# Kernel tuning notes

Measured on AMD Instinct MI355X. Metric: run time of the kernel, lower is better.

Reference implementation:

```python
import jax, jax.numpy as jnp
import numpy as np

# module config (matches init_kwargs)
EMBED = 128; HEADS = 8; HEAD_DIM = EMBED // HEADS  # 16, power of 2
MODES = 16            # hardcoded in FuncSelfAttention
WS = 4                # window_size
SHIFT = 2             # shift_size
NSUB = 8              # n_sub (subdomain grid of the full image)
NW = (NSUB // WS) ** 2   # 4 windows per image
S = WS * WS              # 16 tokens (subdomains) per window
BATCH0 = 4; B = BATCH0 * NW  # 16
P = 32                # per-subdomain spatial resolution (needs P//2+1 >= MODES)
HID = 512             # LogCPB MLP hidden width (Swin-v2 style)


def win_decompose2d(x, nsx, nsy, ws):
    # x: [b, c, H, W] -> [(b*wx*wy), ws*ws, c, sh, sw]
    b, c, H, W = x.shape
    sh = H // nsx; sw = W // nsy
    wx = nsx // ws; wy = nsy // ws
    x = x.reshape(b, c, wx, ws, sh, wy, ws, sw)
    x = x.transpose(0, 2, 5, 3, 6, 1, 4, 7)  # b, wx, wy, qx, qy, c, sh, sw
    return x.reshape(b * wx * wy, ws * ws, c, sh, sw)


def win_recompose2d(x, nsx, nsy, ws):
    # inverse of win_decompose2d: [(b*wx*wy), ws*ws, c, sh, sw] -> [b, c, H, W]
    wx = nsx // ws; wy = nsy // ws
    Bn, s, c, sh, sw = x.shape
    b = Bn // (wx * wy)
    x = x.reshape(b, wx, wy, ws, ws, c, sh, sw)
    x = x.transpose(0, 5, 1, 3, 6, 2, 4, 7)
    return x.reshape(b, c, wx * ws * sh, wy * ws * sw)


def spectral_conv(x, wr, wi):
    # SimpleSpectralConv2d: rfft2 -> low-mode complex channel mixing -> irfft2
    # x: [b, s, cin, h, w]; wr/wi: [cin, cout, m, m]
    m = wr.shape[-1]
    h, w = x.shape[-2:]
    xf = jnp.fft.rfft2(x, axes=(-2, -1))                       # [b,s,cin,h,w//2+1]
    ym = jnp.einsum('bsixy,ioxy->bsoxy', xf[..., :m, :m], wr + 1j * wi)
    out_ft = jnp.zeros(x.shape[:2] + (wr.shape[1], h, w // 2 + 1), dtype=ym.dtype)
    out_ft = out_ft.at[..., :m, :m].set(ym)
    return jnp.fft.irfft2(out_ft, s=(h, w), axes=(-2, -1))


def log_cpb(ws, w1, b1, w2):
    # Swin-v2 style log-spaced continuous position bias MLP -> [heads, S, S]
    g = jnp.arange(ws)
    coords = jnp.stack(jnp.meshgrid(g, g, indexing='ij'), -1).reshape(-1, 2)  # [S,2]
    rel = (coords[:, None, :] - coords[None, :, :]).astype(jnp.float32)       # [S,S,2]
    rel = jnp.sign(rel) * jnp.log2(1.0 + jnp.abs(rel)) / jnp.log2(8.0) * 8.0
    hdn = jax.nn.relu(rel @ w1 + b1)
    return (hdn @ w2).transpose(2, 0, 1)


def _build_attn_mask():
    # Faithful port of the Swin shifted-window mask construction in __init__
    img = np.zeros((NSUB, NSUB), np.float32)
    sl = [slice(0, -WS), slice(-WS, -SHIFT), slice(-SHIFT, None)]
    cnt = 0
    for hs in sl:
        for ws_ in sl:
            img[hs, ws_] = cnt
            cnt += 1
    mw = img.reshape(NSUB // WS, WS, NSUB // WS, WS).transpose(0, 2, 1, 3).reshape(NW, S)
    diff = mw[:, None, :] - mw[:, :, None]
    m = np.where(diff != 0, -1e9, 0.0).astype(np.float32)      # -inf in torch; -1e9 for safe grads
    return np.broadcast_to(m[:, None, :, :], (NW, HEADS, S, S)).copy()


def setup_inputs():
    key = jax.random.key(0)
    ks = jax.random.split(key, 8)
    sc = 1.0 / EMBED
    return {
        'seq': jax.random.normal(ks[0], (B, S, EMBED, P, P), jnp.float32),
        'qkv_wr': jax.random.normal(ks[1], (EMBED, 3 * EMBED, MODES, MODES), jnp.float32) * sc,
        'qkv_wi': jax.random.normal(ks[2], (EMBED, 3 * EMBED, MODES, MODES), jnp.float32) * sc,
        'out_wr': jax.random.normal(ks[3], (EMBED, EMBED, MODES, MODES), jnp.float32) * sc,
        'out_wi': jax.random.normal(ks[4], (EMBED, EMBED, MODES, MODES), jnp.float32) * sc,
        'cpb_w1': jax.random.normal(ks[5], (2, HID), jnp.float32) * 0.1,
        'cpb_b1': jnp.zeros((HID,), jnp.float32),
        'cpb_w2': jax.random.normal(ks[6], (HID, HEADS), jnp.float32) * 0.05,
        'attn_mask': jnp.asarray(_build_attn_mask()),
    }


def reference(seq, qkv_wr, qkv_wi, out_wr, out_wi, cpb_w1, cpb_b1, cpb_w2, attn_mask):
    Bn, s, C, h, w = seq.shape
    ssx = w // WS; ssy = h // WS  # subdomain_size per code: seq.size(-1)//n_sub_x with n_sub_x=window_size
    # shift: recompose windows to images, roll, decompose back
    x = win_recompose2d(seq, WS, WS, WS)
    x = jnp.roll(x, (-SHIFT * ssx, -SHIFT * ssy), axis=(-2, -1))
    x = win_decompose2d(x, WS, WS, WS)
    # qkv = spectral conv + residual tiling (v.repeat with dims[2]=3)
    qkv = spectral_conv(x, qkv_wr, qkv_wi) + jnp.concatenate([x, x, x], axis=2)
    qkv = qkv.reshape(Bn, s, 3, HEADS, HEAD_DIM, h, w)
    q = qkv[:, :, 0].transpose(0, 2, 1, 3, 4, 5)  # [B, H, s, d, h, w]
    k = qkv[:, :, 1].transpose(0, 2, 1, 3, 4, 5)
    v = qkv[:, :, 2].transpose(0, 2, 1, 3, 4, 5)
    bias = attn_mask + log_cpb(WS, cpb_w1, cpb_b1, cpb_w2)[None]  # [nW, H, S, S]
    # 'reimann' scores: Riemann-sum (mean over grid) inner product of q_i, k_j functions
    scale = 1.0 / ((h * w) * jnp.sqrt(jnp.float32(HEAD_DIM)))
    scores = jnp.einsum('bnidxy,bnjdxy->bnij', q, k) * scale      # [B, H, S, S]
    scores = scores.reshape(Bn // NW, NW, HEADS, s, s) + bias[None]
    attn = jax.nn.softmax(scores, axis=-1).reshape(Bn, HEADS, s, s)
    sa = jnp.einsum('bnij,bnjdxy->bnidxy', attn, v)               # [B, H, S, d, h, w]
    sa = sa.transpose(0, 2, 1, 3, 4, 5).reshape(Bn, s, C, h, w)   # _flatten
    sa = spectral_conv(sa, out_wr, out_wi)
    # un-shift
    sa = win_recompose2d(sa, WS, WS, WS)
    sa = jnp.roll(sa, (SHIFT * ssx, SHIFT * ssy), axis=(-2, -1))
    return win_decompose2d(sa, WS, WS, WS)
```

## Files before the change

kernel.cpp:

```cpp
#include <hip/hip_runtime.h>
#include <hip/hip_bf16.h>
#include <math.h>


#define DEVI __device__ __forceinline__
typedef unsigned short u16;
typedef unsigned int u32;
typedef __attribute__((ext_vector_type(8))) short short8;
typedef __attribute__((ext_vector_type(4))) float f32x4;

DEVI u16 f2b(float f) {
  union { __hip_bfloat16 h; u16 u; } cv;
  cv.h = __float2bfloat16(f);
  return cv.u;
}
DEVI float b2f(u16 u) { return __uint_as_float(((u32)u) << 16); }

__global__ __launch_bounds__(256) void k_bias(
    const float* __restrict__ w1, const float* __restrict__ b1,
    const float* __restrict__ w2, const float* __restrict__ amask,
    float* __restrict__ biasb) {
  __shared__ float w1s[1024];
  __shared__ float b1s[512];
  __shared__ float w2s[4096];
  int t = threadIdx.x;
  for (int k = t; k < 1024; k += 256) w1s[k] = w1[k];
  for (int k = t; k < 512; k += 256) b1s[k] = b1[k];
  for (int k = t; k < 4096; k += 256) w2s[k] = w2[k];
  __syncthreads();
  int i = t >> 4, j = t & 15;
  float r0 = (float)((i >> 2) - (j >> 2));
  float r1 = (float)((i & 3) - (j & 3));
  const float sc = 8.0f / 3.0f;
  float f0 = (r0 == 0.f) ? 0.f : copysignf(log2f(1.f + fabsf(r0)) * sc, r0);
  float f1 = (r1 == 0.f) ? 0.f : copysignf(log2f(1.f + fabsf(r1)) * sc, r1);
  float o[8];
#pragma unroll
  for (int h = 0; h < 8; h++) o[h] = 0.f;
  for (int k = 0; k < 512; k++) {
    float hd = f0 * w1s[k] + f1 * w1s[512 + k] + b1s[k];
    hd = fmaxf(hd, 0.f);
#pragma unroll
    for (int h = 0; h < 8; h++) o[h] += hd * w2s[k * 8 + h];
  }
  for (int w = 0; w < 4; w++)
#pragma unroll
    for (int h = 0; h < 8; h++) {
      int idx = ((w * 8 + h) * 16 + i) * 16 + j;
      biasb[idx] = amask[idx] + o[h];
    }
}

__global__ __launch_bounds__(256) void k_transpose_wb(
    const float* __restrict__ wr, const float* __restrict__ wi,
    ushort2* __restrict__ dst, int N) {
  __shared__ ushort2 ld[256][17];
  int t = threadIdx.x;
  int ob = blockIdx.x * 16;
  int cb = blockIdx.y * 8;
  for (int cc = 0; cc < 8; cc++) {
    int c = cb + cc;
    for (int oo = 0; oo < 16; oo++) {
      size_t si = ((size_t)c * N + ob + oo) * 256 + t;
      ushort2 u;
      u.x = f2b(wr[si]);
      u.y = f2b(wi[si]);
      ld[t][oo] = u;
    }
    __syncthreads();
    {
      int oo = t & 15, tq = t >> 4;
#pragma unroll
      for (int mr = 0; mr < 16; mr++) {
        int m = mr * 16 + tq;
        dst[((size_t)m * 128 + c) * N + ob + oo] = ld[m][oo];
      }
    }
    __syncthreads();
  }
}

template <int N>
__global__ __launch_bounds__(256) void k_build_b(
    const ushort2* __restrict__ Ws1, u16* __restrict__ Bt) {
  __shared__ ushort2 tile[128][65];
  int t = threadIdx.x;
  int ob = blockIdx.x;
  int m = blockIdx.y;
  {
    int c4 = t >> 6, o = t & 63;
    for (int cc = 0; cc < 32; cc++) {
      int c = cc * 4 + c4;
      tile[c][o] = Ws1[((size_t)m * 128 + c) * N + ob * 64 + o];
    }
  }
  __syncthreads();
  int l = t & 63, w2 = t >> 6;
  for (int rr = 0; rr < 32; rr++) {
    int r = w2 * 32 + rr;
    int ol = r >> 1, p = r & 1;
    size_t rowoff = ((size_t)m * (2 * N) + (size_t)ob * 128 + r) * 256;
#pragma unroll
    for (int ch = 0; ch < 2; ch++) {
      int c = ch * 64 + l;
      ushort2 wv = tile[c][ol];
      ushort2 u;
      u.x = p ? wv.y : wv.x;
      u.y = p ? wv.x : (u16)(wv.y ^ 0x8000);
      *(ushort2*)(Bt + rowoff + 2 * c) = u;
    }
  }
}

__global__ __launch_bounds__(256) void k_build_wdft(u16* __restrict__ Wdft) {
  int n = blockIdx.x;
  int m = n >> 1, q = n & 1;
  int kx = m >> 4, ky = m & 15;
  int t = threadIdx.x;
#pragma unroll
  for (int i = 0; i < 4; i++) {
    int p = i * 256 + t;
    int u = p >> 5, v = p & 31;
    int ph = (kx * u + ky * v) & 31;
    float th = 6.283185307179586f * (float)ph / 32.f;
    float sv, cv;
    sincosf(th, &sv, &cv);
    Wdft[(size_t)n * 1024 + p] = f2b(q ? -sv : cv);
  }
}

__global__ __launch_bounds__(256) void k_build_widft(u16* __restrict__ Widf) {
  int p = blockIdx.x;
  int x = p >> 5, y = p & 31;
  for (int n = threadIdx.x; n < 512; n += 256) {
    int m = n >> 1, q = n & 1;
    int kx = m >> 4, ky = m & 15;
    int ph = (kx * x + ky * y) & 31;
    float th = 6.283185307179586f * (float)ph / 32.f;
    float sv, cv;
    sincosf(th, &sv, &cv);
    float cky = (ky == 0) ? (1.f / 1024.f) : (2.f / 1024.f);
    Widf[(size_t)p * 512 + n] = f2b(q ? -sv * cky : cv * cky);
  }
}

__global__ __launch_bounds__(256) void k_gather(
    const float* __restrict__ seq, u16* __restrict__ Tbf) {
  int t = threadIdx.x;
  int cq = blockIdx.x;
  int bs = blockIdx.y;
  int b = bs >> 4, s = bs & 15;
  int qx = s >> 2, qy = s & 3;
  int u = t >> 3, vb = (t & 7) * 4;
  int uu = u + 16;
  int u2 = uu & 31;
  int qx2 = (qx + (uu >> 5)) & 3;
  int vv = vb + 16;
  int v2 = vv & 31;
  int qy2 = (qy + (vv >> 5)) & 3;
  int s2 = qx2 * 4 + qy2;
  size_t srcbase = (((size_t)(b * 16 + s2) * 128) << 10) + u2 * 32 + v2;
  size_t dstbase = (((size_t)bs * 128) << 10) + u * 32 + vb;
  for (int cc = 0; cc < 32; cc++) {
    size_t coff = (size_t)(cq * 32 + cc) << 10;
    float4 v = *(const float4*)(seq + srcbase + coff);
    ushort4 o;
    o.x = f2b(v.x);
    o.y = f2b(v.y);
    o.z = f2b(v.z);
    o.w = f2b(v.w);
    *(ushort4*)(Tbf + dstbase + coff) = o;
  }
}

__global__ __launch_bounds__(512) void k_dftm(
    const u16* __restrict__ Wdft, const u16* __restrict__ Tbf,
    float2* __restrict__ Xlow, u16* __restrict__ Xbf) {
  __shared__ char As[32768];
  __shared__ char Bs[16384];
  int t = threadIdx.x;
  int mt = blockIdx.x, bs = blockIdx.y;
  int l = t & 63, w = t >> 6;
  int wm = w >> 1, wn = w & 1;
  f32x4 acc[4][4];
#pragma unroll
  for (int a_ = 0; a_ < 4; a_++)
#pragma unroll
    for (int b_ = 0; b_ < 4; b_++) acc[a_][b_] = (f32x4){0.f, 0.f, 0.f, 0.f};
  const u16* Ab = Wdft + (size_t)mt * 256 * 1024;
  const u16* Bb = Tbf + (size_t)bs * 128 * 1024;
  int srow = t >> 3, ss = t & 7;
  uint4 ra[4], rb[2];
#pragma unroll
  for (int i = 0; i < 4; i++)
    ra[i] = *(const uint4*)(Ab + (size_t)(i * 64 + srow) * 1024 + ss * 8);
#pragma unroll
  for (int i = 0; i < 2; i++)
    rb[i] = *(const uint4*)(Bb + (size_t)(i * 64 + srow) * 1024 + ss * 8);
  for (int kt = 0; kt < 16; kt++) {
    if (kt) __syncthreads();
#pragma unroll
    for (int i = 0; i < 4; i++) {
      int row = i * 64 + srow;
      *(uint4*)(As + row * 128 + ((ss ^ (row & 7)) << 4)) = ra[i];
    }
#pragma unroll
    for (int i = 0; i < 2; i++) {
      int row = i * 64 + srow;
      *(uint4*)(Bs + row * 128 + ((ss ^ (row & 7)) << 4)) = rb[i];
    }
    if (kt < 15) {
#pragma unroll
      for (int i = 0; i < 4; i++)
        ra[i] = *(const uint4*)(Ab + (size_t)(i * 64 + srow) * 1024 +
                                (kt + 1) * 64 + ss * 8);
#pragma unroll
      for (int i = 0; i < 2; i++)
        rb[i] = *(const uint4*)(Bb + (size_t)(i * 64 + srow) * 1024 +
                                (kt + 1) * 64 + ss * 8);
    }
    __syncthreads();
#pragma unroll
    for (int kk = 0; kk < 2; kk++) {
      short8 af[4], bg[4];
#pragma unroll
      for (int fm = 0; fm < 4; fm++) {
        int row = wm * 64 + fm * 16 + (l & 15);
        int chunk = kk * 4 + (l >> 4);
        af[fm] = *(const short8*)(As + row * 128 + ((chunk ^ (row & 7)) << 4));
      }
#pragma unroll
      for (int fn = 0; fn < 4; fn++) {
        int row = wn * 64 + fn * 16 + (l & 15);
        int chunk = kk * 4 + (l >> 4);
        bg[fn] = *(const short8*)(Bs + row * 128 + ((chunk ^ (row & 7)) << 4));
      }
#pragma unroll
      for (int fm = 0; fm < 4; fm++)
#pragma unroll
        for (int fn = 0; fn < 4; fn++)
          acc[fm][fn] = __builtin_amdgcn_mfma_f32_16x16x32_bf16(
              af[fm], bg[fn], acc[fm][fn], 0, 0, 0);
    }
  }
  int cr = (l >> 4) * 4, ccol = l & 15;
#pragma unroll
  for (int fm = 0; fm < 4; fm++) {
    int nbase = mt * 256 + wm * 64 + fm * 16 + cr;
#pragma unroll
    for (int fn = 0; fn < 4; fn++) {
      int c = wn * 64 + fn * 16 + ccol;
#pragma unroll
      for (int rp = 0; rp < 4; rp += 2) {
        int n0 = nbase + rp;
        size_t row = (size_t)(n0 >> 1) * 256 + bs;
        float v0 = acc[fm][fn][rp], v1 = acc[fm][fn][rp + 1];
        Xlow[row * 128 + c] = make_float2(v0, v1);
        ushort2 ub;
        ub.x = f2b(v0);
        ub.y = f2b(v1);
        *(ushort2*)(Xbf + row * 256 + 2 * c) = ub;
      }
    }
  }
}

__global__ __launch_bounds__(64) void k_gram_mfma(
    const u16* __restrict__ Tbf, float* __restrict__ Gpart) {
  int dc = blockIdx.x;
  int bh = blockIdx.y;
  int b = bh >> 3, h = bh & 7;
  int l = threadIdx.x;
  f32x4 a0 = (f32x4){0.f, 0.f, 0.f, 0.f};
  f32x4 a1 = (f32x4){0.f, 0.f, 0.f, 0.f};
  const u16* base =
      Tbf + ((size_t)(b * 16 + (l & 15)) * 128 + h * 16 + dc * 4) * 1024;
  int ko = (l >> 4) * 8;
  for (int kk = 0; kk < 128; kk += 2) {
    short8 f0 = *(const short8*)(base + kk * 32 + ko);
    short8 f1 = *(const short8*)(base + kk * 32 + 32 + ko);
    a0 = __builtin_amdgcn_mfma_f32_16x16x32_bf16(f0, f0, a0, 0, 0, 0);
    a1 = __builtin_amdgcn_mfma_f32_16x16x32_bf16(f1, f1, a1, 0, 0, 0);
  }
  float* dst = Gpart + ((size_t)(dc * 16 + b) * 8 + h) * 256;
#pragma unroll
  for (int r = 0; r < 4; r++)
    dst[((l >> 4) * 4 + r) * 16 + (l & 15)] = a0[r] + a1[r];
}

template <int NP>
__global__ __launch_bounds__(512) void k_mixm(
    const u16* __restrict__ A, const u16* __restrict__ Bm,
    u16* __restrict__ Cb) {
  __shared__ char lds[65536];
  char* As = lds;
  char* Bs = lds + 32768;
  u16* st = (u16*)lds;
  int t = threadIdx.x;
  const int gx = NP / 256;
  int orig = blockIdx.y * gx + blockIdx.x;
  const int tot = gx * 256;
  int lid = (orig & 7) * (tot >> 3) + (orig >> 3);
  int nt = lid % gx;
  int m = lid / gx;
  int l = t & 63, w = t >> 6;
  int wm = w >> 1, wn = w & 1;
  f32x4 acc[4][8];
#pragma unroll
  for (int a_ = 0; a_ < 4; a_++)
#pragma unroll
    for (int b_ = 0; b_ < 8; b_++) acc[a_][b_] = (f32x4){0.f, 0.f, 0.f, 0.f};
  const u16* Ab = A + (size_t)m * 256 * 256;
  const u16* Bb = Bm + ((size_t)m * NP + nt * 256) * 256;
  int srow = t >> 3, ss = t & 7;
  uint4 ra[4], rb[4];
#pragma unroll
  for (int i = 0; i < 4; i++) {
    int row = i * 64 + srow;
    ra[i] = *(const uint4*)(Ab + (size_t)row * 256 + ss * 8);
    rb[i] = *(const uint4*)(Bb + (size_t)row * 256 + ss * 8);
  }
  for (int kt = 0; kt < 4; kt++) {
    if (kt) __syncthreads();
#pragma unroll
    for (int i = 0; i < 4; i++) {
      int row = i * 64 + srow;
      int sw = ((ss ^ (row & 7)) << 4);
      *(uint4*)(As + row * 128 + sw) = ra[i];
      *(uint4*)(Bs + row * 128 + sw) = rb[i];
    }
    if (kt < 3) {
#pragma unroll
      for (int i = 0; i < 4; i++) {
        int row = i * 64 + srow;
        ra[i] =
            *(const uint4*)(Ab + (size_t)row * 256 + (kt + 1) * 64 + ss * 8);
        rb[i] =
            *(const uint4*)(Bb + (size_t)row * 256 + (kt + 1) * 64 + ss * 8);
      }
    }
    __syncthreads();
#pragma unroll
    for (int kk = 0; kk < 2; kk++) {
      short8 af[4], bg[8];
#pragma unroll
      for (int fm = 0; fm < 4; fm++) {
        int row = wm * 64 + fm * 16 + (l & 15);
        int chunk = kk * 4 + (l >> 4);
        af[fm] = *(const short8*)(As + row * 128 + ((chunk ^ (row & 7)) << 4));
      }
#pragma unroll
      for (int fn = 0; fn < 8; fn++) {
        int row = wn * 128 + fn * 16 + (l & 15);
        int chunk = kk * 4 + (l >> 4);
        bg[fn] = *(const short8*)(Bs + row * 128 + ((chunk ^ (row & 7)) << 4));
      }
#pragma unroll
      for (int fm = 0; fm < 4; fm++)
#pragma unroll
        for (int fn = 0; fn < 8; fn++)
          acc[fm][fn] = __builtin_amdgcn_mfma_f32_16x16x32_bf16(
              bg[fn], af[fm], acc[fm][fn], 0, 0, 0);
    }
  }
#pragma unroll
  for (int fm = 0; fm < 4; fm++) {
    __syncthreads();
    int rloc = wm * 16 + (l & 15);
#pragma unroll
    for (int fn = 0; fn < 8; fn++) {
      int col = wn * 128 + fn * 16 + (l >> 4) * 4;
      ushort4 u;
      u.x = f2b(acc[fm][fn][0]);
      u.y = f2b(acc[fm][fn][1]);
      u.z = f2b(acc[fm][fn][2]);
      u.w = f2b(acc[fm][fn][3]);
      *(ushort4*)(st + rloc * 264 + col) = u;
    }
    __syncthreads();
#pragma unroll
    for (int it = 0; it < 4; it++) {
      int idx = it * 512 + t;
      int row = idx >> 5;
      int ch = idx & 31;
      uint4 v = *(const uint4*)(st + row * 264 + ch * 8);
      int bs = (row >> 4) * 64 + fm * 16 + (row & 15);
      *(uint4*)(Cb + ((size_t)m * 256 + bs) * NP + nt * 256 + ch * 8) = v;
    }
  }
}

__global__ __launch_bounds__(256) void k_transp_out(
    const ushort2* __restrict__ OUTb2, ushort2* __restrict__ OUTt2) {
  __shared__ ushort2 ld[128][129];
  int t = threadIdx.x;
  int bs = blockIdx.x;
  for (int mh = 0; mh < 2; mh++) {
    if (mh) __syncthreads();
    {
      int cidx = t & 127;
      int rb = t >> 7;
      for (int pass = 0; pass < 64; pass++) {
        int r = pass * 2 + rb;
        ld[r][cidx] = OUTb2[((size_t)(mh * 128 + r) * 256 + bs) * 128 + cidx];
      }
    }
    __syncthreads();
    {
      int ml = t & 127;
      int cb = t >> 7;
      for (int pass = 0; pass < 64; pass++) {
        int c = pass * 2 + cb;
        OUTt2[((size_t)bs * 128 + c) * 256 + mh * 128 + ml] = ld[ml][c];
      }
    }
  }
}

__global__ __launch_bounds__(512) void k_irfftm(
    const u16* __restrict__ Widf, const u16* __restrict__ OUTt,
    float* __restrict__ tmp) {
  __shared__ char lds[65536];
  char* As = lds;
  char* Bs = lds + 32768;
  float* stg = (float*)lds;
  int t = threadIdx.x;
  int ph = blockIdx.x, bs = blockIdx.y;
  int l = t & 63, w = t >> 6;
  int wm = w >> 1, wn = w & 1;
  f32x4 acc[4][4];
#pragma unroll
  for (int a_ = 0; a_ < 4; a_++)
#pragma unroll
    for (int b_ = 0; b_ < 4; b_++) acc[a_][b_] = (f32x4){0.f, 0.f, 0.f, 0.f};
  const u16* Ab = Widf + (size_t)ph * 256 * 512;
  const u16* Bb = OUTt + (size_t)bs * 128 * 512;
  int srow = t >> 3, ss = t & 7;
  uint4 ra[4], rb[2];
#pragma unroll
  for (int i = 0; i < 4; i++)
    ra[i] = *(const uint4*)(Ab + (size_t)(i * 64 + srow) * 512 + ss * 8);
#pragma unroll
  for (int i = 0; i < 2; i++)
    rb[i] = *(const uint4*)(Bb + (size_t)(i * 64 + srow) * 512 + ss * 8);
  for (int kt = 0; kt < 8; kt++) {
    if (kt) __syncthreads();
#pragma unroll
    for (int i = 0; i < 4; i++) {
      int row = i * 64 + srow;
      *(uint4*)(As + row * 128 + ((ss ^ (row & 7)) << 4)) = ra[i];
    }
#pragma unroll
    for (int i = 0; i < 2; i++) {
      int row = i * 64 + srow;
      *(uint4*)(Bs + row * 128 + ((ss ^ (row & 7)) << 4)) = rb[i];
    }
    if (kt < 7) {
#pragma unroll
      for (int i = 0; i < 4; i++)
        ra[i] = *(const uint4*)(Ab + (size_t)(i * 64 + srow) * 512 +
                                (kt + 1) * 64 + ss * 8);
#pragma unroll
      for (int i = 0; i < 2; i++)
        rb[i] = *(const uint4*)(Bb + (size_t)(i * 64 + srow) * 512 +
                                (kt + 1) * 64 + ss * 8);
    }
    __syncthreads();
#pragma unroll
    for (int kk = 0; kk < 2; kk++) {
      short8 wf[4], bg[4];
#pragma unroll
      for (int fm = 0; fm < 4; fm++) {
        int row = wm * 64 + fm * 16 + (l & 15);
        int chunk = kk * 4 + (l >> 4);
        wf[fm] = *(const short8*)(As + row * 128 + ((chunk ^ (row & 7)) << 4));
      }
#pragma unroll
      for (int fn = 0; fn < 4; fn++) {
        int row = wn * 64 + fn * 16 + (l & 15);
        int chunk = kk * 4 + (l >> 4);
        bg[fn] = *(const short8*)(Bs + row * 128 + ((chunk ^ (row & 7)) << 4));
      }
#pragma unroll
      for (int fm = 0; fm < 4; fm++)
#pragma unroll
        for (int fn = 0; fn < 4; fn++)
          acc[fm][fn] = __builtin_amdgcn_mfma_f32_16x16x32_bf16(
              wf[fm], bg[fn], acc[fm][fn], 0, 0, 0);
    }
  }
  for (int fmp = 0; fmp < 2; fmp++) {
    __syncthreads();
#pragma unroll
    for (int s = 0; s < 2; s++) {
      int fm = fmp * 2 + s;
#pragma unroll
      for (int fn = 0; fn < 4; fn++) {
        int c = wn * 64 + fn * 16 + (l & 15);
        int row = c * 4 + wm;
        int chunk = (s * 4 + (l >> 4)) ^ (c & 7);
        *(float4*)(stg + (row * 8 + chunk) * 4) =
            make_float4(acc[fm][fn][0], acc[fm][fn][1], acc[fm][fn][2],
                        acc[fm][fn][3]);
      }
    }
    __syncthreads();
#pragma unroll
    for (int it = 0; it < 8; it++) {
      int ci = it * 512 + t;
      int row = ci >> 3, k = ci & 7;
      int c = row >> 2, wm2 = row & 3;
      float4 v = *(const float4*)(stg + (row * 8 + (k ^ (c & 7))) * 4);
      int p0 = ph * 256 + wm2 * 64 + fmp * 32 + k * 4;
      *(float4*)(tmp + (((size_t)(bs * 128 + c)) << 10) + p0) = v;
    }
  }
}

__global__ __launch_bounds__(256) void k_unshift(
    const float* __restrict__ tmp, float* __restrict__ out) {
  int t = threadIdx.x;
  int cq = blockIdx.x;
  int bs2 = blockIdx.y;
  int b = bs2 >> 4, s2 = bs2 & 15;
  int qx2 = s2 >> 2, qy2 = s2 & 3;
  int v2 = (t & 7) * 4;
  int y, qy;
  if (v2 < 16) {
    y = v2 + 16;
    qy = (qy2 + 3) & 3;
  } else {
    y = v2 - 16;
    qy = qy2;
  }
  for (int it = 0; it < 32; it++) {
    int row = it * 32 + (t >> 3);
    int c = cq * 32 + (row >> 5);
    int u2 = row & 31;
    int x, qx;
    if (u2 < 16) {
      x = u2 + 16;
      qx = (qx2 + 3) & 3;
    } else {
      x = u2 - 16;
      qx = qx2;
    }
    int bs_src = b * 16 + qx * 4 + qy;
    float4 v = *(const float4*)(tmp + (((size_t)(bs_src * 128 + c)) << 10) +
                                x * 32 + y);
    *(float4*)(out + (((size_t)(bs2 * 128 + c)) << 10) + u2 * 32 + v2) = v;
  }
}

__global__ __launch_bounds__(256) void k_scores(
    const float2* __restrict__ Xlow, const ushort2* __restrict__ QKVmb,
    float* __restrict__ Spart) {
  __shared__ float2 Xs[16][17], Qs[16][17], Ks[16][17];
  int t = threadIdx.x;
  int mc = blockIdx.x;
  int bh = blockIdx.y;
  int b = bh >> 3, h = bh & 7;
  int i = t >> 4, j = t & 15;
  int bs = b * 16 + i;
  int d = j;
  int m0 = mc * 32;
  size_t xoff = ((size_t)m0 * 256 + bs) * 128 + h * 16 + d;
  size_t qoff = ((size_t)m0 * 256 + bs) * 384 + h * 16 + d;
  float2 px = Xlow[xoff];
  ushort2 uq = QKVmb[qoff];
  ushort2 uk = QKVmb[qoff + 128];
  float acc = 0.f;
  for (int mm = 0; mm < 32; mm++) {
    int m = m0 + mm;
    Xs[i][d] = px;
    Qs[i][d] = make_float2(b2f(uq.x), b2f(uq.y));
    Ks[i][d] = make_float2(b2f(uk.x), b2f(uk.y));
    __syncthreads();
    if (mm < 31) {
      px = Xlow[xoff + (size_t)(mm + 1) * 32768];
      uq = QKVmb[qoff + (size_t)(mm + 1) * 98304];
      uk = QKVmb[qoff + (size_t)(mm + 1) * 98304 + 128];
    }
    int ky = m & 15, kx = m >> 4;
    if (ky > 0) {
#pragma unroll
      for (int dd = 0; dd < 16; dd++) {
        float2 Xi = Xs[i][dd], Qi = Qs[i][dd], Xj = Xs[j][dd], Kj = Ks[j][dd];
        float qr = Xi.x + Qi.x, qi = Xi.y + Qi.y;
        float kr = Xj.x + Kj.x, ki = Xj.y + Kj.y;
        acc += 2.f * (qr * kr + qi * ki - (Xi.x * Xj.x + Xi.y * Xj.y));
      }
    } else {
#pragma unroll
      for (int dd = 0; dd < 16; dd++) {
        float2 Xi = Xs[i][dd], Qi = Qs[i][dd], Xj = Xs[j][dd], Kj = Ks[j][dd];
        float cr = Xi.x * Kj.x + Xi.y * Kj.y + Qi.x * Xj.x + Qi.y * Xj.y;
        float qk =
            (kx == 0) ? (Qi.x * Kj.x) : 0.5f * (Qi.x * Kj.x + Qi.y * Kj.y);
        acc += cr + qk;
      }
    }
    __syncthreads();
  }
  Spart[((size_t)mc * 128 + bh) * 256 + t] = acc;
}

__global__ __launch_bounds__(256) void k_softmax(
    const float* __restrict__ Spart, const float* __restrict__ Gpart,
    const float* __restrict__ biasb, float* __restrict__ attn) {
  int t = threadIdx.x;
  int bh = blockIdx.x;
  int b = bh >> 3, h = bh & 7;
  int i = t >> 4, j = t & 15;
  float acc = 0.f;
#pragma unroll
  for (int mc = 0; mc < 8; mc++)
    acc += Spart[((size_t)mc * 128 + bh) * 256 + t];
  float G = 0.f;
#pragma unroll
  for (int dc = 0; dc < 4; dc++)
    G += Gpart[((size_t)(dc * 16 + b) * 8 + h) * 256 + t];
  float score = G * (1.f / 4096.f) + acc * (1.f / 4194304.f) +
                biasb[(((b & 3) * 8 + h) * 16 + i) * 16 + j];
  float mx = score;
#pragma unroll
  for (int o = 8; o >= 1; o >>= 1) mx = fmaxf(mx, __shfl_xor(mx, o, 16));
  float e = expf(score - mx);
  float sm = e;
#pragma unroll
  for (int o = 8; o >= 1; o >>= 1) sm += __shfl_xor(sm, o, 16);
  attn[(size_t)bh * 256 + t] = e / sm;
}

__global__ __launch_bounds__(256) void k_sav(
    const float2* __restrict__ Xlow, const ushort2* __restrict__ QKVmb,
    const float* __restrict__ attn, ushort2* __restrict__ SAfb) {
  __shared__ float at[8][16][17];
  __shared__ float2 vt[16][130];
  int t = threadIdx.x;
  int mc = blockIdx.x;
  int b = blockIdx.y;
  {
    int h = t >> 5, ii = (t >> 1) & 15, jb = (t & 1) * 8;
#pragma unroll
    for (int k = 0; k < 8; k++)
      at[h][ii][jb + k] = attn[((size_t)(b * 8 + h) * 16 + ii) * 16 + jb + k];
  }
  __syncthreads();
  int i = t >> 4, cg = t & 15;
  for (int mm = 0; mm < 16; mm++) {
    int m = mc * 16 + mm;
    int ky = m & 15, kx = m >> 4;
    {
      int jj = t >> 4;
      size_t row = (size_t)m * 256 + b * 16 + jj;
#pragma unroll
      for (int u = 0; u < 8; u++) {
        int c = cg + u * 16;
        ushort2 uv = QKVmb[row * 384 + 256 + c];
        float2 vm = make_float2(b2f(uv.x), b2f(uv.y));
        float2 xv = Xlow[row * 128 + c];
        float2 vh;
        if (ky == 0) {
          if (kx == 0)
            vh = make_float2(xv.x + vm.x, xv.y);
          else
            vh = make_float2(xv.x + 0.5f * vm.x, xv.y + 0.5f * vm.y);
        } else
          vh = make_float2(xv.x + vm.x, xv.y + vm.y);
        vt[jj][c] = vh;
      }
    }
    __syncthreads();
    float2 o8[8];
#pragma unroll
    for (int u = 0; u < 8; u++) o8[u] = make_float2(0.f, 0.f);
#pragma unroll
    for (int jj = 0; jj < 16; jj++) {
#pragma unroll
      for (int u = 0; u < 8; u++) {
        float av = at[u][i][jj];
        float2 v = vt[jj][cg + u * 16];
        o8[u].x += av * v.x;
        o8[u].y += av * v.y;
      }
    }
    size_t orow = (size_t)m * 256 + b * 16 + i;
#pragma unroll
    for (int u = 0; u < 8; u++) {
      ushort2 ub;
      ub.x = f2b(o8[u].x);
      ub.y = f2b(o8[u].y);
      SAfb[orow * 128 + cg + u * 16] = ub;
    }
    __syncthreads();
  }
}

extern "C" void kernel_launch(void* const* d_in, const int* in_sizes, int n_in,
                              void* d_out, int out_size, void* d_ws,
                              size_t ws_size, hipStream_t stream) {
  (void)in_sizes;
  (void)n_in;
  const float* seq = (const float*)d_in[0];
  const float* qwr = (const float*)d_in[1];
  const float* qwi = (const float*)d_in[2];
  const float* owr = (const float*)d_in[3];
  const float* owi = (const float*)d_in[4];
  const float* cw1 = (const float*)d_in[5];
  const float* cb1 = (const float*)d_in[6];
  const float* cw2 = (const float*)d_in[7];
  const float* amask = (const float*)d_in[8];
  float* out = (float*)d_out;
  char* ws = (char*)d_ws;

  const size_t R = 100663296;
  ushort2* Wq_s1b = (ushort2*)ws;
  u16* Tbf = (u16*)ws;
  u16* Xbf = (u16*)(ws + 67108864);
  u16* Wob = (u16*)ws;
  ushort2* QKVmb = (ushort2*)(ws + R);
  u16* OUTb = (u16*)(ws + R);
  u16* OUTt = (u16*)(ws + R + 33554432);
  float* tmpb = (float*)(ws + R + 2 * 33554432);
  u16* Wqb = (u16*)(ws + 2 * R);
  ushort2* SAfb = (ushort2*)(ws + 2 * R);
  ushort2* Wo_s1b = (ushort2*)(ws + 3 * R);
  float2* Xlow = (float2*)(ws + 3 * R + 16777216);
  char* sm = ws + 3 * R + 16777216 + 67108864;
  u16* Wdft = (u16*)sm;
  float* Gpart = (float*)(sm + 1048576);
  float* biasb = (float*)(sm + 1572864);
  float* attn = (float*)(sm + 1605632);
  float* Spart = (float*)(sm + 1736704);
  u16* Widf = (u16*)(sm + 2785280);
  size_t need = 3 * R + 16777216 + 67108864 + 2785280 + 1048576;

  if (ws_size < need) {
    hipMemsetAsync(d_out, 0, (size_t)out_size * 4, stream);
    return;
  }

  dim3 blk(256);
  k_transpose_wb<<<dim3(24, 16), blk, 0, stream>>>(qwr, qwi, Wq_s1b, 384);
  k_build_b<384><<<dim3(6, 256), blk, 0, stream>>>(Wq_s1b, Wqb);
  k_transpose_wb<<<dim3(8, 16), blk, 0, stream>>>(owr, owi, Wo_s1b, 128);
  k_bias<<<dim3(1), blk, 0, stream>>>(cw1, cb1, cw2, amask, biasb);
  k_build_wdft<<<dim3(512), blk, 0, stream>>>(Wdft);
  k_build_widft<<<dim3(1024), blk, 0, stream>>>(Widf);
  k_gather<<<dim3(4, 256), blk, 0, stream>>>(seq, Tbf);
  k_dftm<<<dim3(2, 256), dim3(512), 0, stream>>>(Wdft, Tbf, Xlow, Xbf);
  k_gram_mfma<<<dim3(4, 128), dim3(64), 0, stream>>>(Tbf, Gpart);
  k_mixm<768><<<dim3(3, 256), dim3(512), 0, stream>>>(Xbf, Wqb, (u16*)QKVmb);
  k_scores<<<dim3(8, 128), blk, 0, stream>>>(Xlow, QKVmb, Spart);
  k_softmax<<<dim3(128), blk, 0, stream>>>(Spart, Gpart, biasb, attn);
  k_build_b<128><<<dim3(2, 256), blk, 0, stream>>>(Wo_s1b, Wob);
  k_sav<<<dim3(16, 16), blk, 0, stream>>>(Xlow, QKVmb, attn, SAfb);
  k_mixm<256><<<dim3(1, 256), dim3(512), 0, stream>>>((const u16*)SAfb, Wob,
                                                      OUTb);
  k_transp_out<<<dim3(256), blk, 0, stream>>>((const ushort2*)OUTb,
                                              (ushort2*)OUTt);
  k_irfftm<<<dim3(4, 256), dim3(512), 0, stream>>>(Widf, OUTt, tmpb);
  k_unshift<<<dim3(4, 256), blk, 0, stream>>>(tmpb, out);
}
```

Before: 844.0 us.

## Drop fp32 Xlow buffer and stage DFT output through LDS for coalesced stores

The DFT kernel no longer writes a separate fp32 complex Xlow array. It writes only the bf16 Xbf, staged through shared memory in two passes so global stores become 16-byte coalesced rows. The scores and S·V kernels now read the bf16 copy and convert it on the fly, which cuts write and read traffic for that intermediate. The cost is lower precision for the residual X term in the scores and values, plus extra barriers in the DFT epilogue.

```diff
diff --git a/kernel.cpp b/kernel.cpp
--- a/kernel.cpp
+++ b/kernel.cpp
@@ -175,9 +175,11 @@
 
 __global__ __launch_bounds__(512) void k_dftm(
     const u16* __restrict__ Wdft, const u16* __restrict__ Tbf,
-    float2* __restrict__ Xlow, u16* __restrict__ Xbf) {
-  __shared__ char As[32768];
-  __shared__ char Bs[16384];
+    u16* __restrict__ Xbf) {
+  __shared__ char lds[49152];
+  char* As = lds;
+  char* Bs = lds + 32768;
+  u16* st = (u16*)lds;
   int t = threadIdx.x;
   int mt = blockIdx.x, bs = blockIdx.y;
   int l = t & 63, w = t >> 6;
@@ -244,23 +246,34 @@
     }
   }
   int cr = (l >> 4) * 4, ccol = l & 15;
-#pragma unroll
-  for (int fm = 0; fm < 4; fm++) {
-    int nbase = mt * 256 + wm * 64 + fm * 16 + cr;
-#pragma unroll
-    for (int fn = 0; fn < 4; fn++) {
-      int c = wn * 64 + fn * 16 + ccol;
-#pragma unroll
-      for (int rp = 0; rp < 4; rp += 2) {
-        int n0 = nbase + rp;
-        size_t row = (size_t)(n0 >> 1) * 256 + bs;
-        float v0 = acc[fm][fn][rp], v1 = acc[fm][fn][rp + 1];
-        Xlow[row * 128 + c] = make_float2(v0, v1);
-        ushort2 ub;
-        ub.x = f2b(v0);
-        ub.y = f2b(v1);
-        *(ushort2*)(Xbf + row * 256 + 2 * c) = ub;
-      }
+  for (int pass = 0; pass < 2; pass++) {
+    __syncthreads();
+    if ((wm >> 1) == pass) {
+#pragma unroll
+      for (int fm = 0; fm < 4; fm++) {
+#pragma unroll
+        for (int fn = 0; fn < 4; fn++) {
+          int c = wn * 64 + fn * 16 + ccol;
+#pragma unroll
+          for (int rp = 0; rp < 4; rp += 2) {
+            int rloc = (wm & 1) * 32 + fm * 8 + ((cr + rp) >> 1);
+            ushort2 ub;
+            ub.x = f2b(acc[fm][fn][rp]);
+            ub.y = f2b(acc[fm][fn][rp + 1]);
+            *(ushort2*)(st + rloc * 264 + 2 * c) = ub;
+          }
+        }
+      }
+    }
+    __syncthreads();
+#pragma unroll
+    for (int it = 0; it < 4; it++) {
+      int idx = it * 512 + t;
+      int row = idx >> 5;
+      int ch = idx & 31;
+      uint4 v = *(const uint4*)(st + row * 264 + ch * 8);
+      int m = mt * 128 + pass * 64 + row;
+      *(uint4*)(Xbf + ((size_t)m * 256 + bs) * 256 + ch * 8) = v;
     }
   }
 }
@@ -553,7 +566,7 @@
 }
 
 __global__ __launch_bounds__(256) void k_scores(
-    const float2* __restrict__ Xlow, const ushort2* __restrict__ QKVmb,
+    const ushort2* __restrict__ Xb2, const ushort2* __restrict__ QKVmb,
     float* __restrict__ Spart) {
   __shared__ float2 Xs[16][17], Qs[16][17], Ks[16][17];
   int t = threadIdx.x;
@@ -566,18 +579,18 @@
   int m0 = mc * 32;
   size_t xoff = ((size_t)m0 * 256 + bs) * 128 + h * 16 + d;
   size_t qoff = ((size_t)m0 * 256 + bs) * 384 + h * 16 + d;
-  float2 px = Xlow[xoff];
+  ushort2 ux = Xb2[xoff];
   ushort2 uq = QKVmb[qoff];
   ushort2 uk = QKVmb[qoff + 128];
   float acc = 0.f;
   for (int mm = 0; mm < 32; mm++) {
     int m = m0 + mm;
-    Xs[i][d] = px;
+    Xs[i][d] = make_float2(b2f(ux.x), b2f(ux.y));
     Qs[i][d] = make_float2(b2f(uq.x), b2f(uq.y));
     Ks[i][d] = make_float2(b2f(uk.x), b2f(uk.y));
     __syncthreads();
     if (mm < 31) {
-      px = Xlow[xoff + (size_t)(mm + 1) * 32768];
+      ux = Xb2[xoff + (size_t)(mm + 1) * 32768];
       uq = QKVmb[qoff + (size_t)(mm + 1) * 98304];
       uk = QKVmb[qoff + (size_t)(mm + 1) * 98304 + 128];
     }
@@ -633,7 +646,7 @@
 }
 
 __global__ __launch_bounds__(256) void k_sav(
-    const float2* __restrict__ Xlow, const ushort2* __restrict__ QKVmb,
+    const ushort2* __restrict__ Xb2, const ushort2* __restrict__ QKVmb,
     const float* __restrict__ attn, ushort2* __restrict__ SAfb) {
   __shared__ float at[8][16][17];
   __shared__ float2 vt[16][130];
@@ -659,7 +672,8 @@
         int c = cg + u * 16;
         ushort2 uv = QKVmb[row * 384 + 256 + c];
         float2 vm = make_float2(b2f(uv.x), b2f(uv.y));
-        float2 xv = Xlow[row * 128 + c];
+        ushort2 uxv = Xb2[row * 128 + c];
+        float2 xv = make_float2(b2f(uxv.x), b2f(uxv.y));
         float2 vh;
         if (ky == 0) {
           if (kx == 0)
@@ -718,6 +732,7 @@
   ushort2* Wq_s1b = (ushort2*)ws;
   u16* Tbf = (u16*)ws;
   u16* Xbf = (u16*)(ws + 67108864);
+  ushort2* Xb2 = (ushort2*)Xbf;
   u16* Wob = (u16*)ws;
   ushort2* QKVmb = (ushort2*)(ws + R);
   u16* OUTb = (u16*)(ws + R);
@@ -726,7 +741,6 @@
   u16* Wqb = (u16*)(ws + 2 * R);
   ushort2* SAfb = (ushort2*)(ws + 2 * R);
   ushort2* Wo_s1b = (ushort2*)(ws + 3 * R);
-  float2* Xlow = (float2*)(ws + 3 * R + 16777216);
   char* sm = ws + 3 * R + 16777216 + 67108864;
   u16* Wdft = (u16*)sm;
   float* Gpart = (float*)(sm + 1048576);
@@ -749,13 +763,13 @@
   k_build_wdft<<<dim3(512), blk, 0, stream>>>(Wdft);
   k_build_widft<<<dim3(1024), blk, 0, stream>>>(Widf);
   k_gather<<<dim3(4, 256), blk, 0, stream>>>(seq, Tbf);
-  k_dftm<<<dim3(2, 256), dim3(512), 0, stream>>>(Wdft, Tbf, Xlow, Xbf);
+  k_dftm<<<dim3(2, 256), dim3(512), 0, stream>>>(Wdft, Tbf, Xbf);
   k_gram_mfma<<<dim3(4, 128), dim3(64), 0, stream>>>(Tbf, Gpart);
   k_mixm<768><<<dim3(3, 256), dim3(512), 0, stream>>>(Xbf, Wqb, (u16*)QKVmb);
-  k_scores<<<dim3(8, 128), blk, 0, stream>>>(Xlow, QKVmb, Spart);
+  k_scores<<<dim3(8, 128), blk, 0, stream>>>(Xb2, QKVmb, Spart);
   k_softmax<<<dim3(128), blk, 0, stream>>>(Spart, Gpart, biasb, attn);
   k_build_b<128><<<dim3(2, 256), blk, 0, stream>>>(Wo_s1b, Wob);
-  k_sav<<<dim3(16, 16), blk, 0, stream>>>(Xlow, QKVmb, attn, SAfb);
+  k_sav<<<dim3(16, 16), blk, 0, stream>>>(Xb2, QKVmb, attn, SAfb);
   k_mixm<256><<<dim3(1, 256), dim3(512), 0, stream>>>((const u16*)SAfb, Wob,
                                                       OUTb);
   k_transp_out<<<dim3(256), blk, 0, stream>>>((const ushort2*)OUTb,
```

Result: faster. 820.8 us (-2.8%).
